# Kernel tuning notes

Measured on AMD Instinct MI355X. Metric: run time of the kernel, lower is better.

The kernel has to match this reference:

```python
import jax, jax.numpy as jnp
import numpy as np

B, T, P = 4, 512, 3584          # batch, new tokens per seq, cached tokens per seq
D_MODEL, H, KH, DH = 2048, 16, 4, 128
N_REP = H // KH
MAX_SEQ = 4096
ROPE_BASE = 1e6
EPS = 1e-6


def _rmsnorm(t, w):
    # t: [..., DH]
    var = jnp.mean(t * t, axis=-1, keepdims=True)
    return t * jax.lax.rsqrt(var + EPS) * w


def _rope(t, positions):
    # t: [N, heads, DH], positions: [N] int
    half = DH // 2
    inv_freq = (1.0 / ROPE_BASE) ** (2.0 * jnp.arange(half, dtype=jnp.float32) / DH)
    theta = positions.astype(jnp.float32)[:, None] * inv_freq[None, :]   # [N, half]
    theta = jnp.concatenate([theta, theta], axis=-1)                      # [N, DH]
    sin = jnp.sin(theta)[:, None, :]
    cos = jnp.cos(theta)[:, None, :]
    x1, x2 = jnp.split(t, 2, axis=-1)
    rot = jnp.concatenate([-x2, x1], axis=-1)
    return cos * t + sin * rot


def setup_inputs() -> dict:
    key = jax.random.key(0)
    ks = jax.random.split(key, 9)
    N = B * T
    x = jax.random.normal(ks[0], (N, D_MODEL), dtype=jnp.float32)
    k_cache = jax.random.normal(ks[1], (B, KH, P, DH), dtype=jnp.float32)
    v_cache = jax.random.normal(ks[2], (B, KH, P, DH), dtype=jnp.float32)
    s = 1.0 / np.sqrt(D_MODEL)
    w_q = jax.random.normal(ks[3], (H * DH, D_MODEL), dtype=jnp.float32) * s
    w_k = jax.random.normal(ks[4], (KH * DH, D_MODEL), dtype=jnp.float32) * s
    w_v = jax.random.normal(ks[5], (KH * DH, D_MODEL), dtype=jnp.float32) * s
    w_o = jax.random.normal(ks[6], (D_MODEL, H * DH), dtype=jnp.float32) * s
    q_norm_w = jnp.ones((DH,), dtype=jnp.float32)
    k_norm_w = jnp.ones((DH,), dtype=jnp.float32)
    # each sequence's new tokens occupy absolute positions [P, P+T)
    positions = jnp.tile(P + jnp.arange(T, dtype=jnp.int32), B)  # [B*T]
    return {"x": x, "k_cache": k_cache, "v_cache": v_cache,
            "w_q": w_q, "w_k": w_k, "w_v": w_v, "w_o": w_o,
            "q_norm_w": q_norm_w, "k_norm_w": k_norm_w,
            "positions": positions}


def reference(x, k_cache, v_cache, w_q, w_k, w_v, w_o, q_norm_w, k_norm_w, positions):
    N = x.shape[0]
    # QKV projections (no bias)
    q = (x @ w_q.T).reshape(N, H, DH)
    k = (x @ w_k.T).reshape(N, KH, DH)
    v = (x @ w_v.T).reshape(N, KH, DH)
    # per-head RMSNorm then RoPE at absolute positions
    q = _rope(_rmsnorm(q, q_norm_w), positions)
    k = _rope(_rmsnorm(k, k_norm_w), positions)
    # assemble full KV: cached (pre-rotated) past + new tokens
    k_new = k.reshape(B, T, KH, DH).transpose(0, 2, 1, 3)   # [B,KH,T,DH]
    v_new = v.reshape(B, T, KH, DH).transpose(0, 2, 1, 3)
    k_full = jnp.concatenate([k_cache, k_new], axis=2)       # [B,KH,P+T,DH]
    v_full = jnp.concatenate([v_cache, v_new], axis=2)
    # GQA: repeat each kv head n_rep times
    k_rep = jnp.repeat(k_full, N_REP, axis=1)                # [B,H,S,DH]
    v_rep = jnp.repeat(v_full, N_REP, axis=1)
    q4 = q.reshape(B, T, H, DH).transpose(0, 2, 1, 3)        # [B,H,T,DH]
    scale = 1.0 / jnp.sqrt(jnp.float32(DH))
    scores = jnp.einsum('bhtd,bhsd->bhts', q4, k_rep) * scale  # [B,H,T,P+T]
    # right-bottom causal mask: q_pos = P + t, kv_pos = s
    q_pos = P + jnp.arange(T)
    kv_pos = jnp.arange(P + T)
    mask = q_pos[:, None] >= kv_pos[None, :]
    scores = jnp.where(mask[None, None], scores, -jnp.inf)
    attn = jax.nn.softmax(scores, axis=-1)
    out = jnp.einsum('bhts,bhsd->bhtd', attn, v_rep)          # [B,H,T,DH]
    out = out.transpose(0, 2, 1, 3).reshape(N, H * DH)
    return out @ w_o.T
```

## Files before the change

### kernel.cpp

```cpp
#include <hip/hip_runtime.h>
#include <hip/hip_bf16.h>
#include <stdint.h>

#define B_   4
#define T_   512
#define P_   3584
#define S_   4096
#define H_   16
#define KH_  4
#define DM_  2048
#define DH_  128
#define NTOK 2048
#define NCHUNK 3
#define NROWS 32768

typedef __attribute__((ext_vector_type(8)))  short          bf16x8;
typedef __attribute__((ext_vector_type(4)))  float          f32x4;
typedef __attribute__((ext_vector_type(16))) float          f32x16;
typedef __attribute__((ext_vector_type(4)))  float          f4v;
typedef __attribute__((ext_vector_type(4)))  unsigned short us4v;

__device__ __forceinline__ unsigned short f2bf(float x) {
    union { float f; unsigned u; } v; v.f = x;
    unsigned r = v.u + 0x7FFFu + ((v.u >> 16) & 1u);
    return (unsigned short)(r >> 16);
}
__device__ __forceinline__ float bf2f(unsigned short b) {
    union { unsigned u; float f; } v; v.u = ((unsigned)b) << 16; return v.f;
}
__device__ __forceinline__ unsigned pkbf(float a, float b) {
    __hip_bfloat162 h = __float22bfloat162_rn(float2{a, b});
    union { __hip_bfloat162 h; unsigned u; } cv; cv.h = h; return cv.u;
}
__device__ __forceinline__ float ex2(float x) {
    float r; asm("v_exp_f32 %0, %1" : "=v"(r) : "v"(x)); return r;
}
__device__ __forceinline__ float max3f(float a, float b, float c) {
    float r; asm("v_max3_f32 %0, %1, %2, %3" : "=v"(r) : "v"(a), "v"(b), "v"(c)); return r;
}
__device__ __forceinline__ float sin_rev(float xf) {
    float r; asm("v_sin_f32 %0, %1" : "=v"(r) : "v"(xf)); return r;
}
__device__ __forceinline__ float cos_rev(float xf) {
    float r; asm("v_cos_f32 %0, %1" : "=v"(r) : "v"(xf)); return r;
}

#define GLDS16(gp, lp) __builtin_amdgcn_global_load_lds( \
    (const __attribute__((address_space(1))) void*)(gp), \
    (__attribute__((address_space(3))) void*)(lp), 16, 0, 0)

__global__ __launch_bounds__(256) void convert_all(
    const float* __restrict__ x,  const float* __restrict__ wq,
    const float* __restrict__ wk, const float* __restrict__ wv,
    const float* __restrict__ wo, const float* __restrict__ kc,
    const float* __restrict__ vc,
    unsigned short* __restrict__ xb,   unsigned short* __restrict__ wqkvb,
    unsigned short* __restrict__ wob,  unsigned short* __restrict__ kfull,
    unsigned short* __restrict__ vT)
{
    __shared__ unsigned short tile[64][65];
    if (blockIdx.x >= 2048) {
        const int id = blockIdx.x - 2048;
        const int bk = id / 112;
        const int rem = id % 112;
        const int st = rem >> 1;
        const int dt = rem & 1;
        const float* src = vc + ((size_t)bk * P_ + st * 64) * DH_ + dt * 64;
        const int tq = threadIdx.x & 15;
        const int ts = threadIdx.x >> 4;
        #pragma unroll
        for (int i = 0; i < 4; ++i) {
            const int si = ts + i * 16;
            f4v v = *(const f4v*)(src + (size_t)si * DH_ + tq * 4);
            tile[si][tq*4+0] = f2bf(v[0]); tile[si][tq*4+1] = f2bf(v[1]);
            tile[si][tq*4+2] = f2bf(v[2]); tile[si][tq*4+3] = f2bf(v[3]);
        }
        __syncthreads();
        unsigned short* dst = vT + ((size_t)bk * DH_ + dt * 64) * S_ + st * 64;
        const int sq = threadIdx.x & 15;
        const int td = threadIdx.x >> 4;
        #pragma unroll
        for (int i = 0; i < 4; ++i) {
            const int di = td + i * 16;
            us4v o;
            o[0] = tile[sq*4+0][di]; o[1] = tile[sq*4+1][di];
            o[2] = tile[sq*4+2][di]; o[3] = tile[sq*4+3][di];
            *(us4v*)(dst + (size_t)di * S_ + sq * 4) = o;
        }
        return;
    }
    const long total = 5505024;
    for (long i = (long)blockIdx.x * 256 + threadIdx.x; i < total;
         i += 2048L * 256) {
        const f4v* src; us4v* dst; long s4, d4;
        if (i < 1048576)      { src=(const f4v*)x;  dst=(us4v*)xb;              s4=i;         d4=s4; }
        else if (i < 2097152) { src=(const f4v*)wq; dst=(us4v*)wqkvb;           s4=i-1048576; d4=s4; }
        else if (i < 2359296) { src=(const f4v*)wk; dst=(us4v*)(wqkvb+4194304); s4=i-2097152; d4=s4; }
        else if (i < 2621440) { src=(const f4v*)wv; dst=(us4v*)(wqkvb+5242880); s4=i-2359296; d4=s4; }
        else if (i < 3670016) { src=(const f4v*)wo; dst=(us4v*)wob;             s4=i-2621440; d4=s4; }
        else                  { s4=i-3670016; long bk=s4/114688;
                                d4=bk*131072+(s4-bk*114688);
                                src=(const f4v*)kc; dst=(us4v*)kfull; }
        f4v v = src[s4];
        us4v o; o[0]=f2bf(v[0]); o[1]=f2bf(v[1]); o[2]=f2bf(v[2]); o[3]=f2bf(v[3]);
        dst[d4] = o;
    }
}

__global__ __launch_bounds__(256) void gemm_bt(
    const unsigned short* __restrict__ A, const unsigned short* __restrict__ Bw,
    void* __restrict__ C, int M, int N, int K, int obf16)
{
    __shared__ short As[2][128 * 32];
    __shared__ short Bs[2][128 * 32];
    const int tid = threadIdx.x, lane = tid & 63, w = tid >> 6;
    const int nbn = N >> 7;
    const int cpx = nbn >> 3;
    const int xcd = blockIdx.x & 7;
    const int rr = blockIdx.x >> 3;
    const int bm = rr / cpx, bn = xcd * cpx + rr % cpx;
    const int m0 = bm << 7, n0 = bn << 7;
    const int wm = w >> 1, wn = w & 1;

    f32x4 acc[4][4];
    #pragma unroll
    for (int i = 0; i < 4; ++i)
        #pragma unroll
        for (int j = 0; j < 4; ++j)
            #pragma unroll
            for (int r = 0; r < 4; ++r) acc[i][j][r] = 0.f;

    const int arow = lane >> 2;
    const int acol = (lane & 3) << 3;

    auto stage = [&](int buf, int k0) {
        #pragma unroll
        for (int cc = 0; cc < 2; ++cc) {
            const int c = 2 * w + cc;
            GLDS16(A  + (size_t)(m0 + c * 16 + arow) * K + k0 + acol, &As[buf][c * 512]);
            GLDS16(Bw + (size_t)(n0 + c * 16 + arow) * K + k0 + acol, &Bs[buf][c * 512]);
        }
    };

    stage(0, 0);
    __syncthreads();

    const int nk = K >> 5;
    const int fr = lane & 15, fk = (lane >> 4) << 3;
    for (int t = 0; t < nk; ++t) {
        const int buf = t & 1;
        if (t + 1 < nk) stage(buf ^ 1, (t + 1) << 5);
        bf16x8 a[4], b[4];
        #pragma unroll
        for (int i = 0; i < 4; ++i)
            a[i] = *(const bf16x8*)&As[buf][(wm * 64 + i * 16 + fr) * 32 + fk];
        #pragma unroll
        for (int j = 0; j < 4; ++j)
            b[j] = *(const bf16x8*)&Bs[buf][(wn * 64 + j * 16 + fr) * 32 + fk];
        __builtin_amdgcn_s_setprio(1);
        #pragma unroll
        for (int i = 0; i < 4; ++i)
            #pragma unroll
            for (int j = 0; j < 4; ++j)
                acc[i][j] = __builtin_amdgcn_mfma_f32_16x16x32_bf16(a[i], b[j], acc[i][j], 0, 0, 0);
        __builtin_amdgcn_s_setprio(0);
        __syncthreads();
    }

    const int er = lane >> 4, ec = lane & 15;
    #pragma unroll
    for (int i = 0; i < 4; ++i)
        #pragma unroll
        for (int j = 0; j < 4; ++j)
            #pragma unroll
            for (int r = 0; r < 4; ++r) {
                const int row = m0 + wm * 64 + i * 16 + er * 4 + r;
                const int col = n0 + wn * 64 + j * 16 + ec;
                if (obf16) ((unsigned short*)C)[(size_t)row * N + col] = f2bf(acc[i][j][r]);
                else       ((float*)C)[(size_t)row * N + col] = acc[i][j][r];
            }
}

__global__ __launch_bounds__(256) void norm_rope(
    const unsigned short* __restrict__ qkv, const float* __restrict__ qw,
    const float* __restrict__ kw,  const int* __restrict__ pos,
    unsigned short* __restrict__ Qb, unsigned short* __restrict__ Kf,
    unsigned short* __restrict__ VT)
{
    const int task = blockIdx.x * 4 + (threadIdx.x >> 6);
    const int n = task / 24, idx = task % 24;
    const int lane = threadIdx.x & 63;
    const int b = n >> 9, t = n & 511;

    if (idx >= 20) {
        const int kh = idx - 20;
        const unsigned short* src = qkv + (size_t)n * 3072 + 2560 + kh * 128;
        unsigned short* dstT = VT + (size_t)(b * KH_ + kh) * DH_ * S_ + (P_ + t);
        dstT[(size_t)lane * S_]        = src[lane];
        dstT[(size_t)(lane + 64) * S_] = src[lane + 64];
        return;
    }
    const bool isq = idx < 16;
    const int hh = isq ? idx : (idx - 16);
    const unsigned short* src = qkv + (size_t)n * 3072 + (isq ? hh * 128 : 2048 + hh * 128);
    const float* wn_ = isq ? qw : kw;
    float x0 = bf2f(src[lane]), x1 = bf2f(src[lane + 64]);
    float ss = x0 * x0 + x1 * x1;
    #pragma unroll
    for (int m = 1; m < 64; m <<= 1) ss += __shfl_xor(ss, m);
    const float rinv = rsqrtf(ss * (1.0f / 128.0f) + 1e-6f);
    float y0 = x0 * rinv * wn_[lane];
    float y1 = x1 * rinv * wn_[lane + 64];
    const float fr = ex2(-(float)lane * (19.931568569324174f / 64.0f));
    const float th = (float)pos[n] * fr;
    const float xr = th * 0.15915494309189535f;
    const float xf = xr - floorf(xr);
    const float sn = sin_rev(xf), cs = cos_rev(xf);
    float o0 = cs * y0 - sn * y1;
    float o1 = cs * y1 + sn * y0;
    unsigned short* dst;
    if (isq) {
        const float qs = 0.08838834764831845f * 1.4426950408889634f;
        o0 *= qs; o1 *= qs;
        dst = Qb + ((size_t)(b * H_ + hh) * T_ + t) * DH_;
    } else {
        dst = Kf + ((size_t)(b * KH_ + hh) * S_ + P_ + t) * DH_;
    }
    dst[lane]      = f2bf(o0);
    dst[lane + 64] = f2bf(o1);
}

__global__ __launch_bounds__(256, 3) void attn(
    const unsigned short* __restrict__ Qb, const unsigned short* __restrict__ Kf,
    const unsigned short* __restrict__ VT, unsigned short* __restrict__ op0,
    unsigned short* __restrict__ op1, unsigned short* __restrict__ op2,
    float2* __restrict__ ml)
{
    __shared__ short Ks[3][32 * 128];
    __shared__ short Vs[3][128 * 32];

    const int tid = threadIdx.x, lane = tid & 63, w = tid >> 6;
    const int c = blockIdx.x >> 8;
    const int y = blockIdx.x & 255;
    const int xcd = y & 7, slot = y >> 3;
    const int p = xcd + 8 * (slot >> 4);
    const int inner = slot & 15;
    const int b = p >> 2, kvh = p & 3;
    const int h = kvh * 4 + (inner >> 2);
    const int qt = inner & 3;
    const int t0 = qt * 128;

    const unsigned short* Qrow = Qb + (size_t)(b * H_ + h) * T_ * DH_;
    const unsigned short* Kb   = Kf + (size_t)(b * KH_ + kvh) * S_ * DH_;
    const unsigned short* VTb  = VT + (size_t)(b * KH_ + kvh) * DH_ * S_;

    const int ql = lane & 31;
    const int hi = lane >> 5;

    bf16x8 qf[8];
    {
        const unsigned short* qp = Qrow + (size_t)(t0 + w * 32 + ql) * DH_ + hi * 8;
        #pragma unroll
        for (int d0 = 0; d0 < 8; ++d0) qf[d0] = *(const bf16x8*)(qp + d0 * 16);
    }

    f32x16 o[4];
    #pragma unroll
    for (int d = 0; d < 4; ++d)
        #pragma unroll
        for (int r = 0; r < 16; ++r) o[d][r] = 0.f;
    float m_run = -INFINITY, l_run = 0.f;

    const int q_pos = P_ + t0 + w * 32 + ql;
    const int s_end_wave = P_ + t0 + w * 32 + 32;
    const int nt_full = (P_ + t0 + 128) >> 5;
    const int nj = (nt_full - c + 2) / 3;

    auto stage = [&](int buf, int tile) {
        const int s0 = tile << 5;
        #pragma unroll
        for (int cc = 0; cc < 2; ++cc) {
            const int cx = 2 * w + cc;
            const int krow = cx * 4 + (lane >> 4);
            const int kel  = 8 * ((lane & 15) ^ (krow & 15));
            GLDS16(Kb + (size_t)(s0 + krow) * DH_ + kel, &Ks[buf][cx * 512]);
            const int vrow = cx * 16 + (lane >> 2);
            const int vel  = 8 * ((lane & 3) ^ ((lane >> 3) & 3));
            GLDS16(VTb + (size_t)vrow * S_ + s0 + vel, &Vs[buf][cx * 512]);
        }
    };

    stage(0, c);
    if (nj > 1) stage(1, c + 3);

    for (int j = 0; j < nj; ++j) {
        if (j + 1 < nj) asm volatile("s_waitcnt vmcnt(4)" ::: "memory");
        else            asm volatile("s_waitcnt vmcnt(0)" ::: "memory");
        __builtin_amdgcn_s_barrier();
        if (j + 2 < nj) stage((j + 2) % 3, c + 3 * (j + 2));

        const int t = c + 3 * j;
        const int s0 = t << 5;
        const int buf = j % 3;
        if (s0 < s_end_wave) {
            f32x16 st0, st1;
            #pragma unroll
            for (int r = 0; r < 16; ++r) { st0[r] = 0.f; st1[r] = 0.f; }
            {
                const char* kbase = (const char*)&Ks[buf][0] + ql * 256;
                const int sw = 16 * (ql & 15);
                __builtin_amdgcn_s_setprio(1);
                #pragma unroll
                for (int d0 = 0; d0 < 4; ++d0) {
                    bf16x8 kf0 = *(const bf16x8*)(kbase + ((d0 * 32 + 16 * hi) ^ sw));
                    bf16x8 kf1 = *(const bf16x8*)(kbase + (((d0 + 4) * 32 + 16 * hi) ^ sw));
                    st0 = __builtin_amdgcn_mfma_f32_32x32x16_bf16(kf0, qf[d0], st0, 0, 0, 0);
                    st1 = __builtin_amdgcn_mfma_f32_32x32x16_bf16(kf1, qf[d0 + 4], st1, 0, 0, 0);
                }
                __builtin_amdgcn_s_setprio(0);
            }
            f32x16 st;
            #pragma unroll
            for (int r = 0; r < 16; ++r) st[r] = st0[r] + st1[r];
            if (s0 + 31 > P_ + t0 + w * 32) {
                #pragma unroll
                for (int r = 0; r < 16; ++r) {
                    const int srow = (r & 3) + 8 * (r >> 2) + 4 * hi;
                    if (s0 + srow > q_pos) st[r] = -INFINITY;
                }
            }
            float m0_ = max3f(st[0], st[1], st[2]),  m1_ = max3f(st[3], st[4], st[5]);
            float m2_ = max3f(st[6], st[7], st[8]),  m3_ = max3f(st[9], st[10], st[11]);
            float m4_ = max3f(st[12], st[13], st[14]);
            float pmax = fmaxf(max3f(m0_, m1_, m2_), max3f(m3_, m4_, st[15]));
            pmax = fmaxf(pmax, __shfl_xor(pmax, 32));
            if (!__all(pmax <= m_run + 11.5f)) {
                const float m_new = fmaxf(m_run, pmax);
                const float alpha = ex2(m_run - m_new);
                l_run *= alpha;
                #pragma unroll
                for (int r = 0; r < 16; ++r) {
                    const int qr = (r & 3) + 8 * (r >> 2) + 4 * hi;
                    const float a = __shfl(alpha, qr);
                    #pragma unroll
                    for (int d = 0; d < 4; ++d) o[d][r] *= a;
                }
                m_run = m_new;
            }
            float pv[16]; float psum = 0.f;
            #pragma unroll
            for (int r = 0; r < 16; ++r) { pv[r] = ex2(st[r] - m_run); psum += pv[r]; }
            psum += __shfl_xor(psum, 32);
            l_run += psum;
            unsigned pk[8];
            #pragma unroll
            for (int u = 0; u < 8; ++u) pk[u] = pkbf(pv[2 * u], pv[2 * u + 1]);
            unsigned xw[8];
            #pragma unroll
            for (int u = 0; u < 8; ++u) xw[u] = (unsigned)__shfl_xor((int)pk[u], 32);
            union { bf16x8 v; unsigned u[4]; } pa0, pa1;
            pa0.u[0] = hi ? xw[2] : pk[0];  pa0.u[1] = hi ? xw[3] : pk[1];
            pa0.u[2] = hi ? pk[2] : xw[0];  pa0.u[3] = hi ? pk[3] : xw[1];
            pa1.u[0] = hi ? xw[6] : pk[4];  pa1.u[1] = hi ? xw[7] : pk[5];
            pa1.u[2] = hi ? pk[6] : xw[4];  pa1.u[3] = hi ? pk[7] : xw[5];
            __builtin_amdgcn_s_setprio(1);
            #pragma unroll
            for (int ch = 0; ch < 2; ++ch)
                #pragma unroll
                for (int db = 0; db < 4; ++db) {
                    const int vrow = db * 32 + ql;
                    bf16x8 vf = *(const bf16x8*)&Vs[buf][vrow * 32 + 8 * ((2 * ch + hi) ^ ((ql >> 1) & 3))];
                    o[db] = __builtin_amdgcn_mfma_f32_32x32x16_bf16(
                        ch ? pa1.v : pa0.v, vf, o[db], 0, 0, 0);
                }
            __builtin_amdgcn_s_setprio(0);
        }
    }

    unsigned short* op = (c == 0) ? op0 : (c == 1) ? op1 : op2;
    const int rowbase = (b * H_ + h) * T_ + t0 + w * 32;
    if (hi == 0) ml[c * NROWS + rowbase + ql] = float2{m_run, l_run};
    #pragma unroll
    for (int r = 0; r < 16; ++r) {
        const int qr = (r & 3) + 8 * (r >> 2) + 4 * hi;
        unsigned short* orow = op + (size_t)(rowbase + qr) * DH_;
        #pragma unroll
        for (int d = 0; d < 4; ++d)
            orow[d * 32 + ql] = f2bf(o[d][r]);
    }
}

__global__ __launch_bounds__(256) void combine(
    const float2* __restrict__ ml,
    const unsigned short* __restrict__ op0, const unsigned short* __restrict__ op1,
    const unsigned short* __restrict__ op2, unsigned short* __restrict__ ao)
{
    const int row = blockIdx.x * 4 + (threadIdx.x >> 6);
    const int lane = threadIdx.x & 63;
    const float2 a0 = ml[row], a1 = ml[NROWS + row], a2 = ml[2 * NROWS + row];
    const float m = fmaxf(a0.x, fmaxf(a1.x, a2.x));
    const float w0 = ex2(a0.x - m), w1 = ex2(a1.x - m), w2 = ex2(a2.x - m);
    const float Linv = 1.0f / (w0 * a0.y + w1 * a1.y + w2 * a2.y);
    const size_t src = (size_t)row * DH_ + 2 * lane;
    const unsigned u0 = *(const unsigned*)(op0 + src);
    const unsigned u1 = *(const unsigned*)(op1 + src);
    const unsigned u2 = *(const unsigned*)(op2 + src);
    const float v0 = (bf2f((unsigned short)u0) * w0 + bf2f((unsigned short)u1) * w1 +
                      bf2f((unsigned short)u2) * w2) * Linv;
    const float v1 = (bf2f((unsigned short)(u0 >> 16)) * w0 + bf2f((unsigned short)(u1 >> 16)) * w1 +
                      bf2f((unsigned short)(u2 >> 16)) * w2) * Linv;
    const int t = row & 511, h = (row >> 9) & 15, b = row >> 13;
    unsigned short* dst = ao + ((size_t)(b * T_ + t) * (H_ * DH_)) + h * DH_ + 2 * lane;
    *(unsigned*)dst = pkbf(v0, v1);
}

extern "C" void kernel_launch(void* const* d_in, const int* in_sizes, int n_in,
                              void* d_out, int out_size, void* d_ws, size_t ws_size,
                              hipStream_t stream)
{
    const float* x   = (const float*)d_in[0];
    const float* kc  = (const float*)d_in[1];
    const float* vc  = (const float*)d_in[2];
    const float* wq  = (const float*)d_in[3];
    const float* wk  = (const float*)d_in[4];
    const float* wv  = (const float*)d_in[5];
    const float* wo  = (const float*)d_in[6];
    const float* qnw = (const float*)d_in[7];
    const float* knw = (const float*)d_in[8];
    const int*   pos = (const int*)d_in[9];
    float* out = (float*)d_out;

    char* ws = (char*)d_ws;
    unsigned short* xb    = (unsigned short*)(ws + 0);
    unsigned short* wqkvb = (unsigned short*)(ws + 8388608);
    unsigned short* wob   = (unsigned short*)(ws + 20971520);
    unsigned short* qkvb  = (unsigned short*)(ws + 29360128);
    unsigned short* qb    = (unsigned short*)(ws + 41943040);
    unsigned short* kfull = (unsigned short*)(ws + 50331648);
    unsigned short* vT    = (unsigned short*)(ws + 67108864);
    unsigned short* ao    = (unsigned short*)(ws + 83886080);
    unsigned short* op0   = (unsigned short*)(ws + 0);
    unsigned short* op1   = (unsigned short*)(ws + 8388608);
    float2*         ml    = (float2*)(ws + 16777216);
    unsigned short* op2   = (unsigned short*)(ws + 29360128);

    hipLaunchKernelGGL(convert_all, dim3(2048 + 1792), dim3(256), 0, stream,
                       x, wq, wk, wv, wo, kc, vc, xb, wqkvb, wob, kfull, vT);
    hipLaunchKernelGGL(gemm_bt, dim3(16 * 24), dim3(256), 0, stream,
                       xb, wqkvb, (void*)qkvb, 2048, 3072, 2048, 1);
    hipLaunchKernelGGL(norm_rope, dim3(NTOK * 24 / 4), dim3(256), 0, stream,
                       qkvb, qnw, knw, pos, qb, kfull, vT);
    hipLaunchKernelGGL(attn, dim3(NCHUNK * 256), dim3(256), 0, stream,
                       qb, kfull, vT, op0, op1, op2, ml);
    hipLaunchKernelGGL(combine, dim3(NROWS / 4), dim3(256), 0, stream,
                       ml, op0, op1, op2, ao);
    hipLaunchKernelGGL(gemm_bt, dim3(16 * 16), dim3(256), 0, stream,
                       ao, wob, (void*)out, 2048, 2048, 2048, 0);
}
```

Before: 231.8 us.

## Split attention KV into four chunks with double-buffered LDS and occupancy four

Raises the split-KV chunk count from three to four, giving 1024 attention blocks, and adds a fourth partial output buffer that the combine kernel merges. LDS staging drops from a triple-buffered async pipeline to a double buffer with full __syncthreads barriers, and launch bounds rise to four blocks per SM. QK^T now uses a single MFMA accumulation chain instead of two interleaved chains, and the s_setprio hints are removed. The aim is more parallelism and occupancy. The trade-offs are extra barrier stalls, less prefetch depth, a serial MFMA dependency chain, and more partial-output traffic in combine.

```diff
diff --git a/kernel.cpp b/kernel.cpp
--- a/kernel.cpp
+++ b/kernel.cpp
@@ -11,7 +11,7 @@
 #define DM_  2048
 #define DH_  128
 #define NTOK 2048
-#define NCHUNK 3
+#define NCHUNK 4
 #define NROWS 32768
 
 typedef __attribute__((ext_vector_type(8)))  short          bf16x8;
@@ -230,14 +230,14 @@
     dst[lane + 64] = f2bf(o1);
 }
 
-__global__ __launch_bounds__(256, 3) void attn(
+__global__ __launch_bounds__(256, 4) void attn(
     const unsigned short* __restrict__ Qb, const unsigned short* __restrict__ Kf,
     const unsigned short* __restrict__ VT, unsigned short* __restrict__ op0,
     unsigned short* __restrict__ op1, unsigned short* __restrict__ op2,
-    float2* __restrict__ ml)
-{
-    __shared__ short Ks[3][32 * 128];
-    __shared__ short Vs[3][128 * 32];
+    unsigned short* __restrict__ op3, float2* __restrict__ ml)
+{
+    __shared__ short Ks[2][32 * 128];
+    __shared__ short Vs[2][128 * 32];
 
     const int tid = threadIdx.x, lane = tid & 63, w = tid >> 6;
     const int c = blockIdx.x >> 8;
@@ -274,7 +274,7 @@
     const int q_pos = P_ + t0 + w * 32 + ql;
     const int s_end_wave = P_ + t0 + w * 32 + 32;
     const int nt_full = (P_ + t0 + 128) >> 5;
-    const int nj = (nt_full - c + 2) / 3;
+    const int nj = (nt_full - c + 3) >> 2;
 
     auto stage = [&](int buf, int tile) {
         const int s0 = tile << 5;
@@ -291,37 +291,25 @@
     };
 
     stage(0, c);
-    if (nj > 1) stage(1, c + 3);
+    __syncthreads();
 
     for (int j = 0; j < nj; ++j) {
-        if (j + 1 < nj) asm volatile("s_waitcnt vmcnt(4)" ::: "memory");
-        else            asm volatile("s_waitcnt vmcnt(0)" ::: "memory");
-        __builtin_amdgcn_s_barrier();
-        if (j + 2 < nj) stage((j + 2) % 3, c + 3 * (j + 2));
-
-        const int t = c + 3 * j;
-        const int s0 = t << 5;
-        const int buf = j % 3;
+        const int buf = j & 1;
+        if (j + 1 < nj) stage(buf ^ 1, c + 4 * (j + 1));
+        const int s0 = (c + 4 * j) << 5;
         if (s0 < s_end_wave) {
-            f32x16 st0, st1;
-            #pragma unroll
-            for (int r = 0; r < 16; ++r) { st0[r] = 0.f; st1[r] = 0.f; }
+            f32x16 st;
+            #pragma unroll
+            for (int r = 0; r < 16; ++r) st[r] = 0.f;
             {
                 const char* kbase = (const char*)&Ks[buf][0] + ql * 256;
                 const int sw = 16 * (ql & 15);
-                __builtin_amdgcn_s_setprio(1);
                 #pragma unroll
-                for (int d0 = 0; d0 < 4; ++d0) {
-                    bf16x8 kf0 = *(const bf16x8*)(kbase + ((d0 * 32 + 16 * hi) ^ sw));
-                    bf16x8 kf1 = *(const bf16x8*)(kbase + (((d0 + 4) * 32 + 16 * hi) ^ sw));
-                    st0 = __builtin_amdgcn_mfma_f32_32x32x16_bf16(kf0, qf[d0], st0, 0, 0, 0);
-                    st1 = __builtin_amdgcn_mfma_f32_32x32x16_bf16(kf1, qf[d0 + 4], st1, 0, 0, 0);
+                for (int d0 = 0; d0 < 8; ++d0) {
+                    bf16x8 kfr = *(const bf16x8*)(kbase + ((d0 * 32 + 16 * hi) ^ sw));
+                    st = __builtin_amdgcn_mfma_f32_32x32x16_bf16(kfr, qf[d0], st, 0, 0, 0);
                 }
-                __builtin_amdgcn_s_setprio(0);
             }
-            f32x16 st;
-            #pragma unroll
-            for (int r = 0; r < 16; ++r) st[r] = st0[r] + st1[r];
             if (s0 + 31 > P_ + t0 + w * 32) {
                 #pragma unroll
                 for (int r = 0; r < 16; ++r) {
@@ -347,23 +335,23 @@
                 }
                 m_run = m_new;
             }
-            float pv[16]; float psum = 0.f;
-            #pragma unroll
-            for (int r = 0; r < 16; ++r) { pv[r] = ex2(st[r] - m_run); psum += pv[r]; }
+            float psum = 0.f;
+            #pragma unroll
+            for (int r = 0; r < 16; ++r) { st[r] = ex2(st[r] - m_run); psum += st[r]; }
             psum += __shfl_xor(psum, 32);
             l_run += psum;
             unsigned pk[8];
             #pragma unroll
-            for (int u = 0; u < 8; ++u) pk[u] = pkbf(pv[2 * u], pv[2 * u + 1]);
-            unsigned xw[8];
-            #pragma unroll
-            for (int u = 0; u < 8; ++u) xw[u] = (unsigned)__shfl_xor((int)pk[u], 32);
+            for (int u = 0; u < 8; ++u) pk[u] = pkbf(st[2 * u], st[2 * u + 1]);
             union { bf16x8 v; unsigned u[4]; } pa0, pa1;
-            pa0.u[0] = hi ? xw[2] : pk[0];  pa0.u[1] = hi ? xw[3] : pk[1];
-            pa0.u[2] = hi ? pk[2] : xw[0];  pa0.u[3] = hi ? pk[3] : xw[1];
-            pa1.u[0] = hi ? xw[6] : pk[4];  pa1.u[1] = hi ? xw[7] : pk[5];
-            pa1.u[2] = hi ? pk[6] : xw[4];  pa1.u[3] = hi ? pk[7] : xw[5];
-            __builtin_amdgcn_s_setprio(1);
+            { unsigned xx = (unsigned)__shfl_xor((int)pk[2], 32); pa0.u[0] = hi ? xx : pk[0]; }
+            { unsigned xx = (unsigned)__shfl_xor((int)pk[3], 32); pa0.u[1] = hi ? xx : pk[1]; }
+            { unsigned xx = (unsigned)__shfl_xor((int)pk[0], 32); pa0.u[2] = hi ? pk[2] : xx; }
+            { unsigned xx = (unsigned)__shfl_xor((int)pk[1], 32); pa0.u[3] = hi ? pk[3] : xx; }
+            { unsigned xx = (unsigned)__shfl_xor((int)pk[6], 32); pa1.u[0] = hi ? xx : pk[4]; }
+            { unsigned xx = (unsigned)__shfl_xor((int)pk[7], 32); pa1.u[1] = hi ? xx : pk[5]; }
+            { unsigned xx = (unsigned)__shfl_xor((int)pk[4], 32); pa1.u[2] = hi ? pk[6] : xx; }
+            { unsigned xx = (unsigned)__shfl_xor((int)pk[5], 32); pa1.u[3] = hi ? pk[7] : xx; }
             #pragma unroll
             for (int ch = 0; ch < 2; ++ch)
                 #pragma unroll
@@ -373,11 +361,11 @@
                     o[db] = __builtin_amdgcn_mfma_f32_32x32x16_bf16(
                         ch ? pa1.v : pa0.v, vf, o[db], 0, 0, 0);
                 }
-            __builtin_amdgcn_s_setprio(0);
         }
-    }
-
-    unsigned short* op = (c == 0) ? op0 : (c == 1) ? op1 : op2;
+        __syncthreads();
+    }
+
+    unsigned short* op = (c == 0) ? op0 : (c == 1) ? op1 : (c == 2) ? op2 : op3;
     const int rowbase = (b * H_ + h) * T_ + t0 + w * 32;
     if (hi == 0) ml[c * NROWS + rowbase + ql] = float2{m_run, l_run};
     #pragma unroll
@@ -393,22 +381,26 @@
 __global__ __launch_bounds__(256) void combine(
     const float2* __restrict__ ml,
     const unsigned short* __restrict__ op0, const unsigned short* __restrict__ op1,
-    const unsigned short* __restrict__ op2, unsigned short* __restrict__ ao)
+    const unsigned short* __restrict__ op2, const unsigned short* __restrict__ op3,
+    unsigned short* __restrict__ ao)
 {
     const int row = blockIdx.x * 4 + (threadIdx.x >> 6);
     const int lane = threadIdx.x & 63;
-    const float2 a0 = ml[row], a1 = ml[NROWS + row], a2 = ml[2 * NROWS + row];
-    const float m = fmaxf(a0.x, fmaxf(a1.x, a2.x));
-    const float w0 = ex2(a0.x - m), w1 = ex2(a1.x - m), w2 = ex2(a2.x - m);
-    const float Linv = 1.0f / (w0 * a0.y + w1 * a1.y + w2 * a2.y);
+    const float2 a0 = ml[row], a1 = ml[NROWS + row];
+    const float2 a2 = ml[2 * NROWS + row], a3 = ml[3 * NROWS + row];
+    const float m = fmaxf(fmaxf(a0.x, a1.x), fmaxf(a2.x, a3.x));
+    const float w0 = ex2(a0.x - m), w1 = ex2(a1.x - m);
+    const float w2 = ex2(a2.x - m), w3 = ex2(a3.x - m);
+    const float Linv = 1.0f / (w0 * a0.y + w1 * a1.y + w2 * a2.y + w3 * a3.y);
     const size_t src = (size_t)row * DH_ + 2 * lane;
     const unsigned u0 = *(const unsigned*)(op0 + src);
     const unsigned u1 = *(const unsigned*)(op1 + src);
     const unsigned u2 = *(const unsigned*)(op2 + src);
+    const unsigned u3 = *(const unsigned*)(op3 + src);
     const float v0 = (bf2f((unsigned short)u0) * w0 + bf2f((unsigned short)u1) * w1 +
-                      bf2f((unsigned short)u2) * w2) * Linv;
+                      bf2f((unsigned short)u2) * w2 + bf2f((unsigned short)u3) * w3) * Linv;
     const float v1 = (bf2f((unsigned short)(u0 >> 16)) * w0 + bf2f((unsigned short)(u1 >> 16)) * w1 +
-                      bf2f((unsigned short)(u2 >> 16)) * w2) * Linv;
+                      bf2f((unsigned short)(u2 >> 16)) * w2 + bf2f((unsigned short)(u3 >> 16)) * w3) * Linv;
     const int t = row & 511, h = (row >> 9) & 15, b = row >> 13;
     unsigned short* dst = ao + ((size_t)(b * T_ + t) * (H_ * DH_)) + h * DH_ + 2 * lane;
     *(unsigned*)dst = pkbf(v0, v1);
@@ -443,6 +435,7 @@
     unsigned short* op1   = (unsigned short*)(ws + 8388608);
     float2*         ml    = (float2*)(ws + 16777216);
     unsigned short* op2   = (unsigned short*)(ws + 29360128);
+    unsigned short* op3   = (unsigned short*)(ws + 92274688);
 
     hipLaunchKernelGGL(convert_all, dim3(2048 + 1792), dim3(256), 0, stream,
                        x, wq, wk, wv, wo, kc, vc, xb, wqkvb, wob, kfull, vT);
@@ -451,9 +444,9 @@
     hipLaunchKernelGGL(norm_rope, dim3(NTOK * 24 / 4), dim3(256), 0, stream,
                        qkvb, qnw, knw, pos, qb, kfull, vT);
     hipLaunchKernelGGL(attn, dim3(NCHUNK * 256), dim3(256), 0, stream,
-                       qb, kfull, vT, op0, op1, op2, ml);
+                       qb, kfull, vT, op0, op1, op2, op3, ml);
     hipLaunchKernelGGL(combine, dim3(NROWS / 4), dim3(256), 0, stream,
-                       ml, op0, op1, op2, ao);
+                       ml, op0, op1, op2, op3, ao);
     hipLaunchKernelGGL(gemm_bt, dim3(16 * 16), dim3(256), 0, stream,
                        ao, wob, (void*)out, 2048, 2048, 2048, 0);
 }
```

Result: slower. 308.3 us (+33.0%).

## Split-K the QKV projection GEMM and simplify attention QK accumulation

Applied to the files above, without the earlier changes.

The QKV GEMM now runs with split-K over two halves, doubling the grid from 384 to 768 blocks so more CUs are busy. Each half writes a separate bf16 partial, and norm_rope sums the two partials on load. Because the partials are rounded to bf16 before they are added, this adds some rounding error and extra memory traffic. In the attention kernel, the two interleaved QK accumulators are merged into one MFMA chain, s_setprio hints are removed, and the P-matrix shuffles are interleaved with the selects to reduce register pressure.

```diff
diff --git a/kernel.cpp b/kernel.cpp
--- a/kernel.cpp
+++ b/kernel.cpp
@@ -109,15 +109,19 @@
 
 __global__ __launch_bounds__(256) void gemm_bt(
     const unsigned short* __restrict__ A, const unsigned short* __restrict__ Bw,
-    void* __restrict__ C, int M, int N, int K, int obf16)
+    void* __restrict__ C, int M, int N, int K, int obf16, int ksplit)
 {
     __shared__ short As[2][128 * 32];
     __shared__ short Bs[2][128 * 32];
     const int tid = threadIdx.x, lane = tid & 63, w = tid >> 6;
+    int bid = blockIdx.x, ks = 0;
+    if (ksplit) { const int half = gridDim.x >> 1; ks = bid >= half; bid -= ks * half; }
+    const int Ksl = ksplit ? (K >> 1) : K;
+    const int k0base = ks * Ksl;
     const int nbn = N >> 7;
     const int cpx = nbn >> 3;
-    const int xcd = blockIdx.x & 7;
-    const int rr = blockIdx.x >> 3;
+    const int xcd = bid & 7;
+    const int rr = bid >> 3;
     const int bm = rr / cpx, bn = xcd * cpx + rr % cpx;
     const int m0 = bm << 7, n0 = bn << 7;
     const int wm = w >> 1, wn = w & 1;
@@ -142,14 +146,14 @@
         }
     };
 
-    stage(0, 0);
+    stage(0, k0base);
     __syncthreads();
 
-    const int nk = K >> 5;
+    const int nk = Ksl >> 5;
     const int fr = lane & 15, fk = (lane >> 4) << 3;
     for (int t = 0; t < nk; ++t) {
         const int buf = t & 1;
-        if (t + 1 < nk) stage(buf ^ 1, (t + 1) << 5);
+        if (t + 1 < nk) stage(buf ^ 1, k0base + ((t + 1) << 5));
         bf16x8 a[4], b[4];
         #pragma unroll
         for (int i = 0; i < 4; ++i)
@@ -168,6 +172,7 @@
     }
 
     const int er = lane >> 4, ec = lane & 15;
+    const size_t cbase = (size_t)ks * M * N;
     #pragma unroll
     for (int i = 0; i < 4; ++i)
         #pragma unroll
@@ -176,14 +181,15 @@
             for (int r = 0; r < 4; ++r) {
                 const int row = m0 + wm * 64 + i * 16 + er * 4 + r;
                 const int col = n0 + wn * 64 + j * 16 + ec;
-                if (obf16) ((unsigned short*)C)[(size_t)row * N + col] = f2bf(acc[i][j][r]);
-                else       ((float*)C)[(size_t)row * N + col] = acc[i][j][r];
+                if (obf16) ((unsigned short*)C)[cbase + (size_t)row * N + col] = f2bf(acc[i][j][r]);
+                else       ((float*)C)[cbase + (size_t)row * N + col] = acc[i][j][r];
             }
 }
 
 __global__ __launch_bounds__(256) void norm_rope(
-    const unsigned short* __restrict__ qkv, const float* __restrict__ qw,
-    const float* __restrict__ kw,  const int* __restrict__ pos,
+    const unsigned short* __restrict__ qkv0, const unsigned short* __restrict__ qkv1,
+    const float* __restrict__ qw, const float* __restrict__ kw,
+    const int* __restrict__ pos,
     unsigned short* __restrict__ Qb, unsigned short* __restrict__ Kf,
     unsigned short* __restrict__ VT)
 {
@@ -194,17 +200,22 @@
 
     if (idx >= 20) {
         const int kh = idx - 20;
-        const unsigned short* src = qkv + (size_t)n * 3072 + 2560 + kh * 128;
+        const size_t off = (size_t)n * 3072 + 2560 + kh * 128;
+        const unsigned short* s0_ = qkv0 + off;
+        const unsigned short* s1_ = qkv1 + off;
         unsigned short* dstT = VT + (size_t)(b * KH_ + kh) * DH_ * S_ + (P_ + t);
-        dstT[(size_t)lane * S_]        = src[lane];
-        dstT[(size_t)(lane + 64) * S_] = src[lane + 64];
+        dstT[(size_t)lane * S_]        = f2bf(bf2f(s0_[lane]) + bf2f(s1_[lane]));
+        dstT[(size_t)(lane + 64) * S_] = f2bf(bf2f(s0_[lane + 64]) + bf2f(s1_[lane + 64]));
         return;
     }
     const bool isq = idx < 16;
     const int hh = isq ? idx : (idx - 16);
-    const unsigned short* src = qkv + (size_t)n * 3072 + (isq ? hh * 128 : 2048 + hh * 128);
+    const size_t off = (size_t)n * 3072 + (isq ? hh * 128 : 2048 + hh * 128);
+    const unsigned short* s0_ = qkv0 + off;
+    const unsigned short* s1_ = qkv1 + off;
     const float* wn_ = isq ? qw : kw;
-    float x0 = bf2f(src[lane]), x1 = bf2f(src[lane + 64]);
+    float x0 = bf2f(s0_[lane]) + bf2f(s1_[lane]);
+    float x1 = bf2f(s0_[lane + 64]) + bf2f(s1_[lane + 64]);
     float ss = x0 * x0 + x1 * x1;
     #pragma unroll
     for (int m = 1; m < 64; m <<= 1) ss += __shfl_xor(ss, m);
@@ -303,25 +314,18 @@
         const int s0 = t << 5;
         const int buf = j % 3;
         if (s0 < s_end_wave) {
-            f32x16 st0, st1;
-            #pragma unroll
-            for (int r = 0; r < 16; ++r) { st0[r] = 0.f; st1[r] = 0.f; }
+            f32x16 st;
+            #pragma unroll
+            for (int r = 0; r < 16; ++r) st[r] = 0.f;
             {
                 const char* kbase = (const char*)&Ks[buf][0] + ql * 256;
                 const int sw = 16 * (ql & 15);
-                __builtin_amdgcn_s_setprio(1);
                 #pragma unroll
-                for (int d0 = 0; d0 < 4; ++d0) {
-                    bf16x8 kf0 = *(const bf16x8*)(kbase + ((d0 * 32 + 16 * hi) ^ sw));
-                    bf16x8 kf1 = *(const bf16x8*)(kbase + (((d0 + 4) * 32 + 16 * hi) ^ sw));
-                    st0 = __builtin_amdgcn_mfma_f32_32x32x16_bf16(kf0, qf[d0], st0, 0, 0, 0);
-                    st1 = __builtin_amdgcn_mfma_f32_32x32x16_bf16(kf1, qf[d0 + 4], st1, 0, 0, 0);
+                for (int d0 = 0; d0 < 8; ++d0) {
+                    bf16x8 kfr = *(const bf16x8*)(kbase + ((d0 * 32 + 16 * hi) ^ sw));
+                    st = __builtin_amdgcn_mfma_f32_32x32x16_bf16(kfr, qf[d0], st, 0, 0, 0);
                 }
-                __builtin_amdgcn_s_setprio(0);
             }
-            f32x16 st;
-            #pragma unroll
-            for (int r = 0; r < 16; ++r) st[r] = st0[r] + st1[r];
             if (s0 + 31 > P_ + t0 + w * 32) {
                 #pragma unroll
                 for (int r = 0; r < 16; ++r) {
@@ -347,23 +351,23 @@
                 }
                 m_run = m_new;
             }
-            float pv[16]; float psum = 0.f;
-            #pragma unroll
-            for (int r = 0; r < 16; ++r) { pv[r] = ex2(st[r] - m_run); psum += pv[r]; }
+            float psum = 0.f;
+            #pragma unroll
+            for (int r = 0; r < 16; ++r) { st[r] = ex2(st[r] - m_run); psum += st[r]; }
             psum += __shfl_xor(psum, 32);
             l_run += psum;
             unsigned pk[8];
             #pragma unroll
-            for (int u = 0; u < 8; ++u) pk[u] = pkbf(pv[2 * u], pv[2 * u + 1]);
-            unsigned xw[8];
-            #pragma unroll
-            for (int u = 0; u < 8; ++u) xw[u] = (unsigned)__shfl_xor((int)pk[u], 32);
+            for (int u = 0; u < 8; ++u) pk[u] = pkbf(st[2 * u], st[2 * u + 1]);
             union { bf16x8 v; unsigned u[4]; } pa0, pa1;
-            pa0.u[0] = hi ? xw[2] : pk[0];  pa0.u[1] = hi ? xw[3] : pk[1];
-            pa0.u[2] = hi ? pk[2] : xw[0];  pa0.u[3] = hi ? pk[3] : xw[1];
-            pa1.u[0] = hi ? xw[6] : pk[4];  pa1.u[1] = hi ? xw[7] : pk[5];
-            pa1.u[2] = hi ? pk[6] : xw[4];  pa1.u[3] = hi ? pk[7] : xw[5];
-            __builtin_amdgcn_s_setprio(1);
+            { unsigned xx = (unsigned)__shfl_xor((int)pk[2], 32); pa0.u[0] = hi ? xx : pk[0]; }
+            { unsigned xx = (unsigned)__shfl_xor((int)pk[3], 32); pa0.u[1] = hi ? xx : pk[1]; }
+            { unsigned xx = (unsigned)__shfl_xor((int)pk[0], 32); pa0.u[2] = hi ? pk[2] : xx; }
+            { unsigned xx = (unsigned)__shfl_xor((int)pk[1], 32); pa0.u[3] = hi ? pk[3] : xx; }
+            { unsigned xx = (unsigned)__shfl_xor((int)pk[6], 32); pa1.u[0] = hi ? xx : pk[4]; }
+            { unsigned xx = (unsigned)__shfl_xor((int)pk[7], 32); pa1.u[1] = hi ? xx : pk[5]; }
+            { unsigned xx = (unsigned)__shfl_xor((int)pk[4], 32); pa1.u[2] = hi ? pk[6] : xx; }
+            { unsigned xx = (unsigned)__shfl_xor((int)pk[5], 32); pa1.u[3] = hi ? pk[7] : xx; }
             #pragma unroll
             for (int ch = 0; ch < 2; ++ch)
                 #pragma unroll
@@ -373,7 +377,6 @@
                     o[db] = __builtin_amdgcn_mfma_f32_32x32x16_bf16(
                         ch ? pa1.v : pa0.v, vf, o[db], 0, 0, 0);
                 }
-            __builtin_amdgcn_s_setprio(0);
         }
     }
 
@@ -434,26 +437,27 @@
     unsigned short* xb    = (unsigned short*)(ws + 0);
     unsigned short* wqkvb = (unsigned short*)(ws + 8388608);
     unsigned short* wob   = (unsigned short*)(ws + 20971520);
-    unsigned short* qkvb  = (unsigned short*)(ws + 29360128);
-    unsigned short* qb    = (unsigned short*)(ws + 41943040);
-    unsigned short* kfull = (unsigned short*)(ws + 50331648);
-    unsigned short* vT    = (unsigned short*)(ws + 67108864);
-    unsigned short* ao    = (unsigned short*)(ws + 83886080);
+    unsigned short* qkvp0 = (unsigned short*)(ws + 29360128);
+    unsigned short* qkvp1 = (unsigned short*)(ws + 41943040);
+    unsigned short* qb    = (unsigned short*)(ws + 54525952);
+    unsigned short* kfull = (unsigned short*)(ws + 62914560);
+    unsigned short* vT    = (unsigned short*)(ws + 79691776);
     unsigned short* op0   = (unsigned short*)(ws + 0);
     unsigned short* op1   = (unsigned short*)(ws + 8388608);
     float2*         ml    = (float2*)(ws + 16777216);
     unsigned short* op2   = (unsigned short*)(ws + 29360128);
+    unsigned short* ao    = (unsigned short*)(ws + 37748736);
 
     hipLaunchKernelGGL(convert_all, dim3(2048 + 1792), dim3(256), 0, stream,
                        x, wq, wk, wv, wo, kc, vc, xb, wqkvb, wob, kfull, vT);
-    hipLaunchKernelGGL(gemm_bt, dim3(16 * 24), dim3(256), 0, stream,
-                       xb, wqkvb, (void*)qkvb, 2048, 3072, 2048, 1);
+    hipLaunchKernelGGL(gemm_bt, dim3(2 * 16 * 24), dim3(256), 0, stream,
+                       xb, wqkvb, (void*)qkvp0, 2048, 3072, 2048, 1, 1);
     hipLaunchKernelGGL(norm_rope, dim3(NTOK * 24 / 4), dim3(256), 0, stream,
-                       qkvb, qnw, knw, pos, qb, kfull, vT);
+                       qkvp0, qkvp1, qnw, knw, pos, qb, kfull, vT);
     hipLaunchKernelGGL(attn, dim3(NCHUNK * 256), dim3(256), 0, stream,
                        qb, kfull, vT, op0, op1, op2, ml);
     hipLaunchKernelGGL(combine, dim3(NROWS / 4), dim3(256), 0, stream,
                        ml, op0, op1, op2, ao);
     hipLaunchKernelGGL(gemm_bt, dim3(16 * 16), dim3(256), 0, stream,
-                       ao, wob, (void*)out, 2048, 2048, 2048, 0);
-}
+                       ao, wob, (void*)out, 2048, 2048, 2048, 0, 0);
+}
```

Measured after the change: 219.5 us. 5.3% less time.
